# Kernel tuning notes

Measured on AMD Instinct MI355X. Metric: run time of the kernel, lower is better.

## Reference

```python
import jax, jax.numpy as jnp
import numpy as np

IN_DIM = 1024
QK_DIM = 64
NHEADS = 12
HN_MULT = 4
BATCH = 2
SEQ = 2048
BETA = 1.0 / np.sqrt(QK_DIM)


def setup_inputs() -> dict:
    key = jax.random.key(0)
    kg, kq, kk, kw = jax.random.split(key, 4)
    scale = 1.0 / np.sqrt(IN_DIM)
    g = jax.random.normal(kg, (BATCH, SEQ, IN_DIM), dtype=jnp.float32)
    Wq = jax.random.normal(kq, (NHEADS, QK_DIM, IN_DIM), dtype=jnp.float32) * scale
    Wk = jax.random.normal(kk, (NHEADS, QK_DIM, IN_DIM), dtype=jnp.float32) * scale
    Whn = jax.random.normal(kw, (HN_MULT * IN_DIM, IN_DIM), dtype=jnp.float32) * scale
    return {"g": g, "Wq": Wq, "Wk": Wk, "Whn": Whn}


def reference(g, Wq, Wk, Whn):
    # --- attention energy (Energy Transformer): E = -(1/beta) * sum logsumexp_keys(beta * q.k)
    q = jnp.einsum("bnd,hkd->bhnk", g, Wq)  # [B,H,N,K]
    k = jnp.einsum("bnd,hkd->bhnk", g, Wk)  # [B,H,N,K]
    scores = BETA * jnp.einsum("bhnk,bhmk->bhnm", q, k)  # [B,H,N(query),M(key)]
    e_attn = -(1.0 / BETA) * jnp.sum(jax.nn.logsumexp(scores, axis=-1))
    # --- Hopfield energy: -0.5 * sum(relu(W g)^2)
    h = jnp.einsum("bnd,md->bnm", g, Whn)  # [B,N,4*D]
    e_hn = -0.5 * jnp.sum(jax.nn.relu(h) ** 2)
    return e_attn + e_hn
```

## Files before the change

kernel.cpp:

```cpp
#include <hip/hip_runtime.h>
#include <hip/hip_bf16.h>

typedef __attribute__((ext_vector_type(4))) float f32x4;
typedef __attribute__((ext_vector_type(8))) short bf16x8;
typedef unsigned short u16;
typedef __attribute__((ext_vector_type(4))) u16 u16x4;


#define OFF_GB    ((size_t)0)
#define OFF_WQB   ((size_t)8388608)
#define OFF_WKB   ((size_t)(8388608+1572864))
#define OFF_WHNB  ((size_t)(8388608+2*1572864))
#define OFF_QB    (OFF_WHNB + 8388608)
#define OFF_KB    (OFF_QB + 6291456)

__device__ __forceinline__ u16 f2bf(float f) {
  union { float f; unsigned u; } x; x.f = f;
  unsigned u = x.u;
  u += 0x7fffu + ((u >> 16) & 1u);
  return (u16)(u >> 16);
}

__global__ __launch_bounds__(256) void convert_all(
    const float* __restrict__ g, const float* __restrict__ wq,
    const float* __restrict__ wk, const float* __restrict__ whn,
    u16* __restrict__ gB, u16* __restrict__ wqB, u16* __restrict__ wkB, u16* __restrict__ whnB)
{
  const int NG = 1048576;
  const int NW = 196608;
  const int total = NG + 2 * NW + NG;
  for (int i = blockIdx.x * blockDim.x + threadIdx.x; i < total; i += gridDim.x * blockDim.x) {
    const float4* src; u16* dst; int j; float scale = 1.0f;
    if (i < NG)              { src = (const float4*)g;   dst = gB;   j = i; }
    else if (i < NG + NW)    { src = (const float4*)wq;  dst = wqB;  j = i - NG;
                               scale = 0.125f * 1.44269504089f; }
    else if (i < NG + 2*NW)  { src = (const float4*)wk;  dst = wkB;  j = i - NG - NW; }
    else                     { src = (const float4*)whn; dst = whnB; j = i - NG - 2*NW; }
    float4 v = src[j];
    u16x4 o;
    o.x = f2bf(v.x * scale); o.y = f2bf(v.y * scale);
    o.z = f2bf(v.z * scale); o.w = f2bf(v.w * scale);
    *(u16x4*)(dst + (size_t)j * 4) = o;
  }
}

__global__ __launch_bounds__(256) void gemm_bt(
    const u16* __restrict__ A, const u16* __restrict__ B0, const u16* __restrict__ B1,
    u16* __restrict__ C0, u16* __restrict__ C1, int K)
{
  __shared__ u16 lA[128 * 64];
  __shared__ u16 lB[128 * 64];
  const int tid = threadIdx.x;
  const int lane = tid & 63;
  const int w = tid >> 6;
  const int bid = blockIdx.x;
  const int xcd = bid & 7, idx = bid >> 3;
  const int bm = ((xcd >> 1) << 3) + (idx & 7);
  const int bn = (xcd & 1) * 6 + (idx >> 3);

  const u16* Bp; u16* Cp; int bcol0;
  if (bn < 6) { Bp = B0; Cp = C0; bcol0 = bn * 128; }
  else        { Bp = B1; Cp = C1; bcol0 = (bn - 6) * 128; }
  const int arow0 = bm * 128;
  const int wr = w >> 1, wc = w & 1;
  const int l15 = lane & 15, lg = lane >> 4;

  f32x4 acc[4][4];
  const f32x4 zz = {0.f, 0.f, 0.f, 0.f};
#pragma unroll
  for (int m = 0; m < 4; m++)
#pragma unroll
    for (int n = 0; n < 4; n++) acc[m][n] = zz;

#define STAGE(KT) do {                                                                     \
    _Pragma("unroll")                                                                      \
    for (int i = 0; i < 4; i++) {                                                          \
      int rloc = w * 32 + i * 8 + (lane >> 3);                                             \
      int cb   = (((lane & 7) ^ (rloc & 7)) << 4);                                         \
      const char* srcA = (const char*)A + (((size_t)(arow0 + rloc)) * K + (KT) * 64) * 2 + cb; \
      __builtin_amdgcn_global_load_lds((const __attribute__((address_space(1))) void*)srcA, \
          (__attribute__((address_space(3))) void*)((char*)lA + (w * 32 + i * 8) * 128), 16, 0, 0); \
      const char* srcB = (const char*)Bp + (((size_t)(bcol0 + rloc)) * K + (KT) * 64) * 2 + cb; \
      __builtin_amdgcn_global_load_lds((const __attribute__((address_space(1))) void*)srcB, \
          (__attribute__((address_space(3))) void*)((char*)lB + (w * 32 + i * 8) * 128), 16, 0, 0); \
    }                                                                                      \
  } while (0)

  STAGE(0);
  const int nkt = K / 64;
  for (int kt = 0; kt < nkt; ++kt) {
    __syncthreads();
    bf16x8 a0[4], a1[4], b0[4], b1[4];
#pragma unroll
    for (int m = 0; m < 4; m++) {
      int row = wr * 64 + m * 16 + l15;
      const char* base = (const char*)lA + row * 128;
      int sw = (row & 7) << 4;
      a0[m] = *(const bf16x8*)(base + ((lg * 16) ^ sw));
      a1[m] = *(const bf16x8*)(base + ((64 + lg * 16) ^ sw));
    }
#pragma unroll
    for (int n = 0; n < 4; n++) {
      int row = wc * 64 + n * 16 + l15;
      const char* base = (const char*)lB + row * 128;
      int sw = (row & 7) << 4;
      b0[n] = *(const bf16x8*)(base + ((lg * 16) ^ sw));
      b1[n] = *(const bf16x8*)(base + ((64 + lg * 16) ^ sw));
    }
    __syncthreads();
    if (kt + 1 < nkt) STAGE(kt + 1);
#pragma unroll
    for (int m = 0; m < 4; m++)
#pragma unroll
      for (int n = 0; n < 4; n++) {
        acc[m][n] = __builtin_amdgcn_mfma_f32_16x16x32_bf16(a0[m], b0[n], acc[m][n], 0, 0, 0);
        acc[m][n] = __builtin_amdgcn_mfma_f32_16x16x32_bf16(a1[m], b1[n], acc[m][n], 0, 0, 0);
      }
  }
#pragma unroll
  for (int m = 0; m < 4; m++)
#pragma unroll
    for (int n = 0; n < 4; n++)
#pragma unroll
      for (int r = 0; r < 4; r++) {
        int row = arow0 + wr * 64 + m * 16 + lg * 4 + r;
        int col = bcol0 + wc * 64 + n * 16 + l15;
        size_t dst = ((((size_t)(row >> 11) * 12 + (col >> 6)) << 11) + (row & 2047)) * 64 + (col & 63);
        Cp[dst] = f2bf(acc[m][n][r]);
      }
#undef STAGE
}

__global__ __launch_bounds__(512, 2) void hop_gemm8(
    const u16* __restrict__ A, const u16* __restrict__ Bm, float* __restrict__ out)
{
  __shared__ __align__(16) u16 lds[2][2][2][128][64];
  const int tid = threadIdx.x;
  const int lane = tid & 63, w = tid >> 6;
  const int wr = w >> 2, wc = w & 3;
  const int l15 = lane & 15, lg = lane >> 4;
  const int bid = blockIdx.x;
  const int xcd = bid & 7, idx = bid >> 3;
  const int am0 = (((xcd >> 1) << 2) + (idx & 3)) * 256;
  const int bn0 = (((xcd & 1) << 3) + (idx >> 2)) * 256;
  constexpr int nkt = 16;

  f32x4 acc[8][4];
  const f32x4 zz = {0.f, 0.f, 0.f, 0.f};
#pragma unroll
  for (int i = 0; i < 8; i++)
#pragma unroll
    for (int j = 0; j < 4; j++) acc[i][j] = zz;

#define HSTAGE(KT, MAT, H) do {                                                            \
    const u16* s_ = (MAT) ? Bm : A;                                                        \
    int rb_ = ((MAT) ? bn0 : am0) + (H) * 128;                                             \
    char* d0_ = (char*)&lds[(KT) & 1][(MAT)][(H)][0][0];                                   \
    _Pragma("unroll")                                                                      \
    for (int q_ = 0; q_ < 2; q_++) {                                                       \
      int r_ = q_ * 64 + (tid >> 3);                                                       \
      int cb_ = ((tid & 7) * 16) ^ ((r_ & 7) << 4);                                        \
      const char* g_ = (const char*)s_ + (size_t)(rb_ + r_) * 2048 + (KT) * 128 + cb_;     \
      __builtin_amdgcn_global_load_lds((const __attribute__((address_space(1))) void*)g_,  \
          (__attribute__((address_space(3))) void*)(d0_ + q_ * 8192 + tid * 16), 16, 0, 0);\
    }                                                                                      \
  } while (0)

#define LDA_F(DST, P, I, S) do {                                                           \
    int rh_ = ((I) & 3) * 32 + wr * 16 + l15;                                              \
    const char* b_ = (const char*)&lds[(P)][0][(I) >> 2][0][0] + rh_ * 128;                \
    DST = *(const bf16x8*)(b_ + (((S) * 64 + lg * 16) ^ ((rh_ & 7) << 4)));                \
  } while (0)
#define LDB_F(DST, P, J, S) do {                                                           \
    int rh_ = ((J) & 1) * 64 + wc * 16 + l15;                                              \
    const char* b_ = (const char*)&lds[(P)][1][(J) >> 1][0][0] + rh_ * 128;                \
    DST = *(const bf16x8*)(b_ + (((S) * 64 + lg * 16) ^ ((rh_ & 7) << 4)));                \
  } while (0)

  HSTAGE(0, 0, 0); HSTAGE(0, 1, 0); HSTAGE(0, 1, 1); HSTAGE(0, 0, 1);
  HSTAGE(1, 0, 0); HSTAGE(1, 1, 0); HSTAGE(1, 1, 1);
  asm volatile("s_waitcnt vmcnt(6)" ::: "memory");
  __builtin_amdgcn_s_barrier();

  bf16x8 af[4][2], bf[4][2];

#pragma unroll 2
  for (int t = 0; t < nkt; ++t) {
    const int p = t & 1;
#pragma unroll
    for (int m = 0; m < 4; m++) { LDA_F(af[m][0], p, m, 0); LDA_F(af[m][1], p, m, 1); }
#pragma unroll
    for (int n = 0; n < 2; n++) { LDB_F(bf[n][0], p, n, 0); LDB_F(bf[n][1], p, n, 1); }
    if (t + 1 < nkt) HSTAGE(t + 1, 0, 1);
    __builtin_amdgcn_s_barrier();
    __builtin_amdgcn_s_setprio(1);
#pragma unroll
    for (int m = 0; m < 4; m++)
#pragma unroll
      for (int n = 0; n < 2; n++) {
        acc[m][n] = __builtin_amdgcn_mfma_f32_16x16x32_bf16(af[m][0], bf[n][0], acc[m][n], 0, 0, 0);
        acc[m][n] = __builtin_amdgcn_mfma_f32_16x16x32_bf16(af[m][1], bf[n][1], acc[m][n], 0, 0, 0);
      }
    __builtin_amdgcn_s_setprio(0);
    __builtin_amdgcn_s_barrier();
#pragma unroll
    for (int n = 2; n < 4; n++) { LDB_F(bf[n][0], p, n, 0); LDB_F(bf[n][1], p, n, 1); }
    if (t + 2 < nkt) HSTAGE(t + 2, 0, 0);
    __builtin_amdgcn_s_barrier();
    __builtin_amdgcn_s_setprio(1);
#pragma unroll
    for (int m = 0; m < 4; m++)
#pragma unroll
      for (int n = 2; n < 4; n++) {
        acc[m][n] = __builtin_amdgcn_mfma_f32_16x16x32_bf16(af[m][0], bf[n][0], acc[m][n], 0, 0, 0);
        acc[m][n] = __builtin_amdgcn_mfma_f32_16x16x32_bf16(af[m][1], bf[n][1], acc[m][n], 0, 0, 0);
      }
    __builtin_amdgcn_s_setprio(0);
    __builtin_amdgcn_s_barrier();
#pragma unroll
    for (int m = 0; m < 4; m++) { LDA_F(af[m][0], p, m + 4, 0); LDA_F(af[m][1], p, m + 4, 1); }
    if (t + 2 < nkt) HSTAGE(t + 2, 1, 0);
    __builtin_amdgcn_s_barrier();
    __builtin_amdgcn_s_setprio(1);
#pragma unroll
    for (int m = 0; m < 4; m++)
#pragma unroll
      for (int n = 2; n < 4; n++) {
        acc[m + 4][n] = __builtin_amdgcn_mfma_f32_16x16x32_bf16(af[m][0], bf[n][0], acc[m + 4][n], 0, 0, 0);
        acc[m + 4][n] = __builtin_amdgcn_mfma_f32_16x16x32_bf16(af[m][1], bf[n][1], acc[m + 4][n], 0, 0, 0);
      }
    __builtin_amdgcn_s_setprio(0);
    __builtin_amdgcn_s_barrier();
    if (t + 2 < nkt) HSTAGE(t + 2, 1, 1);
    __builtin_amdgcn_s_barrier();
    __builtin_amdgcn_s_setprio(1);
#pragma unroll
    for (int m = 0; m < 4; m++)
#pragma unroll
      for (int n = 0; n < 2; n++) {
        acc[m + 4][n] = __builtin_amdgcn_mfma_f32_16x16x32_bf16(af[m][0], bf[n][0], acc[m + 4][n], 0, 0, 0);
        acc[m + 4][n] = __builtin_amdgcn_mfma_f32_16x16x32_bf16(af[m][1], bf[n][1], acc[m + 4][n], 0, 0, 0);
      }
    __builtin_amdgcn_s_setprio(0);
    if (t < nkt - 2)       asm volatile("s_waitcnt vmcnt(6)" ::: "memory");
    else if (t == nkt - 2) asm volatile("s_waitcnt vmcnt(0)" ::: "memory");
    __builtin_amdgcn_s_barrier();
  }
#undef HSTAGE
#undef LDA_F
#undef LDB_F

  float loc = 0.f;
#pragma unroll
  for (int i = 0; i < 8; i++)
#pragma unroll
    for (int j = 0; j < 4; j++)
#pragma unroll
      for (int r = 0; r < 4; r++) {
        float v = acc[i][j][r];
        loc += (v > 0.f) ? v * v : 0.f;
      }
#pragma unroll
  for (int mask = 32; mask; mask >>= 1) loc += __shfl_xor(loc, mask, 64);
  if (lane == 0) atomicAdd(out, -0.5f * loc);
}

__global__ __launch_bounds__(256) void scores_lse(
    const u16* __restrict__ qB, const u16* __restrict__ kB, float* __restrict__ out)
{
  __shared__ __align__(16) u16 kbuf[3][128 * 64];
  const int z  = blockIdx.x;
  const int qt = blockIdx.y;
  const int tid = threadIdx.x, lane = tid & 63, w = tid >> 6;
  const int l15 = lane & 15, lg = lane >> 4;

  const u16* qp = qB + ((size_t)z * 2048 + qt * 64 + w * 16 + l15) * 64 + lg * 8;
  bf16x8 qf0 = *(const bf16x8*)qp;
  bf16x8 qf1 = *(const bf16x8*)(qp + 32);

#define KSTAGE(KB, BUF) do {                                                               \
    _Pragma("unroll")                                                                      \
    for (int i = 0; i < 4; i++) {                                                          \
      int rloc = i * 32 + w * 8 + (lane >> 3);                                             \
      int cb   = (((lane & 7) ^ (rloc & 7)) << 4);                                         \
      const char* src = (const char*)kB + ((size_t)z * 2048 + (KB) * 128 + rloc) * 128 + cb; \
      __builtin_amdgcn_global_load_lds((const __attribute__((address_space(1))) void*)src,  \
          (__attribute__((address_space(3))) void*)((char*)kbuf[(BUF)] + rloc * 128 + (lane & 7) * 16), 16, 0, 0); \
    }                                                                                      \
  } while (0)

  f32x4 sacc = {0.f, 0.f, 0.f, 0.f};
  const f32x4 zz = {0.f, 0.f, 0.f, 0.f};

  KSTAGE(0, 0);
  KSTAGE(1, 1);
  asm volatile("s_waitcnt vmcnt(4)" ::: "memory");
  __builtin_amdgcn_s_barrier();
  __builtin_amdgcn_sched_barrier(0);

  const int NKB = 16;
  for (int kb = 0; kb < NKB; ++kb) {
    if (kb + 2 < NKB) KSTAGE(kb + 2, (kb + 2) % 3);
    const char* cur = (const char*)kbuf[kb % 3];
#pragma unroll
    for (int g2 = 0; g2 < 8; ++g2) {
      int row = g2 * 16 + l15;
      const char* base = cur + row * 128;
      int sw = (row & 7) << 4;
      bf16x8 b0 = *(const bf16x8*)(base + ((lg * 16) ^ sw));
      bf16x8 b1 = *(const bf16x8*)(base + ((64 + lg * 16) ^ sw));
      f32x4 s = zz;
      s = __builtin_amdgcn_mfma_f32_16x16x32_bf16(qf0, b0, s, 0, 0, 0);
      s = __builtin_amdgcn_mfma_f32_16x16x32_bf16(qf1, b1, s, 0, 0, 0);
      sacc[0] += __builtin_amdgcn_exp2f(s[0]);
      sacc[1] += __builtin_amdgcn_exp2f(s[1]);
      sacc[2] += __builtin_amdgcn_exp2f(s[2]);
      sacc[3] += __builtin_amdgcn_exp2f(s[3]);
    }
    if (kb + 1 < NKB) {
      if (kb + 2 < NKB) asm volatile("s_waitcnt vmcnt(4)" ::: "memory");
      else              asm volatile("s_waitcnt vmcnt(0)" ::: "memory");
      __builtin_amdgcn_s_barrier();
      __builtin_amdgcn_sched_barrier(0);
    }
  }
#undef KSTAGE

#pragma unroll
  for (int mask = 8; mask; mask >>= 1) {
    sacc[0] += __shfl_xor(sacc[0], mask, 64);
    sacc[1] += __shfl_xor(sacc[1], mask, 64);
    sacc[2] += __shfl_xor(sacc[2], mask, 64);
    sacc[3] += __shfl_xor(sacc[3], mask, 64);
  }
  float part = 0.f;
  if (l15 == 0) {
    part = __builtin_amdgcn_logf(sacc[0]) + __builtin_amdgcn_logf(sacc[1]) +
           __builtin_amdgcn_logf(sacc[2]) + __builtin_amdgcn_logf(sacc[3]);
  }
  part += __shfl_xor(part, 16, 64);
  part += __shfl_xor(part, 32, 64);
  if (lane == 0) atomicAdd(out, -5.5451774444795625f * part);
}

extern "C" void kernel_launch(void* const* d_in, const int* in_sizes, int n_in,
                              void* d_out, int out_size, void* d_ws, size_t ws_size,
                              hipStream_t stream)
{
  const float* g   = (const float*)d_in[0];
  const float* Wq  = (const float*)d_in[1];
  const float* Wk  = (const float*)d_in[2];
  const float* Whn = (const float*)d_in[3];
  float* out = (float*)d_out;
  char* ws = (char*)d_ws;

  u16* gB   = (u16*)(ws + OFF_GB);
  u16* wqB  = (u16*)(ws + OFF_WQB);
  u16* wkB  = (u16*)(ws + OFF_WKB);
  u16* whnB = (u16*)(ws + OFF_WHNB);
  u16* qB   = (u16*)(ws + OFF_QB);
  u16* kB   = (u16*)(ws + OFF_KB);

  (void)hipMemsetAsync(out, 0, sizeof(float), stream);

  convert_all<<<2048, 256, 0, stream>>>(g, Wq, Wk, Whn, gB, wqB, wkB, whnB);
  gemm_bt<<<384, 256, 0, stream>>>(gB, wqB, wkB, qB, kB, 1024);
  hop_gemm8<<<256, 512, 0, stream>>>(gB, whnB, out);
  scores_lse<<<dim3(24, 32), 256, 0, stream>>>(qB, kB, out);
}
```

Before: 205.6 us.

## Restructure Hopfield GEMM to 256x128 tiles with 3-stage single-barrier pipeline

Replaces the 256x256 tile, 8-wave ping-pong Hopfield GEMM with a 256x128 tile using K-step 32 and a triple-buffered LDS ring with one barrier per iteration. The grid doubles to 512 blocks and each wave holds half as many accumulators, so launch bounds ask for 4 blocks per CU. The aim is to cut barrier overhead and raise occupancy to hide latency. In exchange, arithmetic intensity per block drops and global/L2 traffic for A roughly doubles.

```diff
diff --git a/kernel.cpp b/kernel.cpp
--- a/kernel.cpp
+++ b/kernel.cpp
@@ -131,133 +131,91 @@
 #undef STAGE
 }
 
-__global__ __launch_bounds__(512, 2) void hop_gemm8(
+__global__ __launch_bounds__(512, 4) void hop_gemm(
     const u16* __restrict__ A, const u16* __restrict__ Bm, float* __restrict__ out)
 {
-  __shared__ __align__(16) u16 lds[2][2][2][128][64];
+  __shared__ __align__(16) u16 lds[3][(256 + 128) * 32];
   const int tid = threadIdx.x;
   const int lane = tid & 63, w = tid >> 6;
-  const int wr = w >> 2, wc = w & 3;
+  const int wr = w >> 1, wc = w & 1;
   const int l15 = lane & 15, lg = lane >> 4;
   const int bid = blockIdx.x;
   const int xcd = bid & 7, idx = bid >> 3;
   const int am0 = (((xcd >> 1) << 2) + (idx & 3)) * 256;
-  const int bn0 = (((xcd & 1) << 3) + (idx >> 2)) * 256;
-  constexpr int nkt = 16;
-
-  f32x4 acc[8][4];
+  const int bn0 = (((xcd & 1) << 4) + (idx >> 2)) * 128;
+  constexpr int nkt = 32;
+
+  f32x4 acc[4][4];
   const f32x4 zz = {0.f, 0.f, 0.f, 0.f};
 #pragma unroll
-  for (int i = 0; i < 8; i++)
-#pragma unroll
-    for (int j = 0; j < 4; j++) acc[i][j] = zz;
-
-#define HSTAGE(KT, MAT, H) do {                                                            \
-    const u16* s_ = (MAT) ? Bm : A;                                                        \
-    int rb_ = ((MAT) ? bn0 : am0) + (H) * 128;                                             \
-    char* d0_ = (char*)&lds[(KT) & 1][(MAT)][(H)][0][0];                                   \
+  for (int m = 0; m < 4; m++)
+#pragma unroll
+    for (int n = 0; n < 4; n++) acc[m][n] = zz;
+
+#define HSTAGE(KT) do {                                                                    \
+    char* s0_ = (char*)&lds[(KT) % 3][0];                                                  \
     _Pragma("unroll")                                                                      \
-    for (int q_ = 0; q_ < 2; q_++) {                                                       \
-      int r_ = q_ * 64 + (tid >> 3);                                                       \
-      int cb_ = ((tid & 7) * 16) ^ ((r_ & 7) << 4);                                        \
-      const char* g_ = (const char*)s_ + (size_t)(rb_ + r_) * 2048 + (KT) * 128 + cb_;     \
+    for (int i_ = 0; i_ < 2; i_++) {                                                       \
+      int r_ = i_ * 128 + (tid >> 2);                                                      \
+      int cb_ = ((tid & 3) * 16) ^ ((r_ & 3) << 4);                                        \
+      const char* g_ = (const char*)A + (size_t)(am0 + r_) * 2048 + (KT) * 64 + cb_;       \
       __builtin_amdgcn_global_load_lds((const __attribute__((address_space(1))) void*)g_,  \
-          (__attribute__((address_space(3))) void*)(d0_ + q_ * 8192 + tid * 16), 16, 0, 0);\
+          (__attribute__((address_space(3))) void*)(s0_ + i_ * 8192 + tid * 16), 16, 0, 0);\
     }                                                                                      \
-  } while (0)
-
-#define LDA_F(DST, P, I, S) do {                                                           \
-    int rh_ = ((I) & 3) * 32 + wr * 16 + l15;                                              \
-    const char* b_ = (const char*)&lds[(P)][0][(I) >> 2][0][0] + rh_ * 128;                \
-    DST = *(const bf16x8*)(b_ + (((S) * 64 + lg * 16) ^ ((rh_ & 7) << 4)));                \
-  } while (0)
-#define LDB_F(DST, P, J, S) do {                                                           \
-    int rh_ = ((J) & 1) * 64 + wc * 16 + l15;                                              \
-    const char* b_ = (const char*)&lds[(P)][1][(J) >> 1][0][0] + rh_ * 128;                \
-    DST = *(const bf16x8*)(b_ + (((S) * 64 + lg * 16) ^ ((rh_ & 7) << 4)));                \
-  } while (0)
-
-  HSTAGE(0, 0, 0); HSTAGE(0, 1, 0); HSTAGE(0, 1, 1); HSTAGE(0, 0, 1);
-  HSTAGE(1, 0, 0); HSTAGE(1, 1, 0); HSTAGE(1, 1, 1);
-  asm volatile("s_waitcnt vmcnt(6)" ::: "memory");
+    {                                                                                      \
+      int r_ = tid >> 2;                                                                   \
+      int cb_ = ((tid & 3) * 16) ^ ((r_ & 3) << 4);                                        \
+      const char* g_ = (const char*)Bm + (size_t)(bn0 + r_) * 2048 + (KT) * 64 + cb_;      \
+      __builtin_amdgcn_global_load_lds((const __attribute__((address_space(1))) void*)g_,  \
+          (__attribute__((address_space(3))) void*)(s0_ + 16384 + tid * 16), 16, 0, 0);    \
+    }                                                                                      \
+  } while (0)
+
+#define LDA2(DST, SL, M) do {                                                              \
+    int r_ = wr * 64 + (M) * 16 + l15;                                                     \
+    DST = *(const bf16x8*)((const char*)&lds[(SL)][0] + r_ * 64 + ((lg * 16) ^ ((r_ & 3) << 4))); \
+  } while (0)
+#define LDB2(DST, SL, N) do {                                                              \
+    int r_ = wc * 64 + (N) * 16 + l15;                                                     \
+    DST = *(const bf16x8*)((const char*)&lds[(SL)][0] + 16384 + r_ * 64 + ((lg * 16) ^ ((r_ & 3) << 4))); \
+  } while (0)
+
+  HSTAGE(0);
+  HSTAGE(1);
+  asm volatile("s_waitcnt vmcnt(3)" ::: "memory");
   __builtin_amdgcn_s_barrier();
 
-  bf16x8 af[4][2], bf[4][2];
-
-#pragma unroll 2
   for (int t = 0; t < nkt; ++t) {
-    const int p = t & 1;
-#pragma unroll
-    for (int m = 0; m < 4; m++) { LDA_F(af[m][0], p, m, 0); LDA_F(af[m][1], p, m, 1); }
-#pragma unroll
-    for (int n = 0; n < 2; n++) { LDB_F(bf[n][0], p, n, 0); LDB_F(bf[n][1], p, n, 1); }
-    if (t + 1 < nkt) HSTAGE(t + 1, 0, 1);
-    __builtin_amdgcn_s_barrier();
+    const int sl = t % 3;
+    if (t + 2 < nkt) HSTAGE(t + 2);
+    bf16x8 av[4], bv[4];
+#pragma unroll
+    for (int m = 0; m < 4; m++) LDA2(av[m], sl, m);
+#pragma unroll
+    for (int n = 0; n < 4; n++) LDB2(bv[n], sl, n);
     __builtin_amdgcn_s_setprio(1);
 #pragma unroll
     for (int m = 0; m < 4; m++)
 #pragma unroll
-      for (int n = 0; n < 2; n++) {
-        acc[m][n] = __builtin_amdgcn_mfma_f32_16x16x32_bf16(af[m][0], bf[n][0], acc[m][n], 0, 0, 0);
-        acc[m][n] = __builtin_amdgcn_mfma_f32_16x16x32_bf16(af[m][1], bf[n][1], acc[m][n], 0, 0, 0);
-      }
+      for (int n = 0; n < 4; n++)
+        acc[m][n] = __builtin_amdgcn_mfma_f32_16x16x32_bf16(av[m], bv[n], acc[m][n], 0, 0, 0);
     __builtin_amdgcn_s_setprio(0);
-    __builtin_amdgcn_s_barrier();
-#pragma unroll
-    for (int n = 2; n < 4; n++) { LDB_F(bf[n][0], p, n, 0); LDB_F(bf[n][1], p, n, 1); }
-    if (t + 2 < nkt) HSTAGE(t + 2, 0, 0);
-    __builtin_amdgcn_s_barrier();
-    __builtin_amdgcn_s_setprio(1);
-#pragma unroll
-    for (int m = 0; m < 4; m++)
-#pragma unroll
-      for (int n = 2; n < 4; n++) {
-        acc[m][n] = __builtin_amdgcn_mfma_f32_16x16x32_bf16(af[m][0], bf[n][0], acc[m][n], 0, 0, 0);
-        acc[m][n] = __builtin_amdgcn_mfma_f32_16x16x32_bf16(af[m][1], bf[n][1], acc[m][n], 0, 0, 0);
-      }
-    __builtin_amdgcn_s_setprio(0);
-    __builtin_amdgcn_s_barrier();
-#pragma unroll
-    for (int m = 0; m < 4; m++) { LDA_F(af[m][0], p, m + 4, 0); LDA_F(af[m][1], p, m + 4, 1); }
-    if (t + 2 < nkt) HSTAGE(t + 2, 1, 0);
-    __builtin_amdgcn_s_barrier();
-    __builtin_amdgcn_s_setprio(1);
-#pragma unroll
-    for (int m = 0; m < 4; m++)
-#pragma unroll
-      for (int n = 2; n < 4; n++) {
-        acc[m + 4][n] = __builtin_amdgcn_mfma_f32_16x16x32_bf16(af[m][0], bf[n][0], acc[m + 4][n], 0, 0, 0);
-        acc[m + 4][n] = __builtin_amdgcn_mfma_f32_16x16x32_bf16(af[m][1], bf[n][1], acc[m + 4][n], 0, 0, 0);
-      }
-    __builtin_amdgcn_s_setprio(0);
-    __builtin_amdgcn_s_barrier();
-    if (t + 2 < nkt) HSTAGE(t + 2, 1, 1);
-    __builtin_amdgcn_s_barrier();
-    __builtin_amdgcn_s_setprio(1);
-#pragma unroll
-    for (int m = 0; m < 4; m++)
-#pragma unroll
-      for (int n = 0; n < 2; n++) {
-        acc[m + 4][n] = __builtin_amdgcn_mfma_f32_16x16x32_bf16(af[m][0], bf[n][0], acc[m + 4][n], 0, 0, 0);
-        acc[m + 4][n] = __builtin_amdgcn_mfma_f32_16x16x32_bf16(af[m][1], bf[n][1], acc[m + 4][n], 0, 0, 0);
-      }
-    __builtin_amdgcn_s_setprio(0);
-    if (t < nkt - 2)       asm volatile("s_waitcnt vmcnt(6)" ::: "memory");
-    else if (t == nkt - 2) asm volatile("s_waitcnt vmcnt(0)" ::: "memory");
-    __builtin_amdgcn_s_barrier();
+    if (t + 2 < nkt)      asm volatile("s_waitcnt vmcnt(3)" ::: "memory");
+    else if (t + 1 < nkt) asm volatile("s_waitcnt vmcnt(0)" ::: "memory");
+    if (t + 1 < nkt) __builtin_amdgcn_s_barrier();
   }
 #undef HSTAGE
-#undef LDA_F
-#undef LDB_F
+#undef LDA2
+#undef LDB2
 
   float loc = 0.f;
 #pragma unroll
-  for (int i = 0; i < 8; i++)
-#pragma unroll
-    for (int j = 0; j < 4; j++)
+  for (int m = 0; m < 4; m++)
+#pragma unroll
+    for (int n = 0; n < 4; n++)
 #pragma unroll
       for (int r = 0; r < 4; r++) {
-        float v = acc[i][j][r];
+        float v = acc[m][n][r];
         loc += (v > 0.f) ? v * v : 0.f;
       }
 #pragma unroll
@@ -365,6 +323,6 @@
 
   convert_all<<<2048, 256, 0, stream>>>(g, Wq, Wk, Whn, gB, wqB, wkB, whnB);
   gemm_bt<<<384, 256, 0, stream>>>(gB, wqB, wkB, qB, kB, 1024);
-  hop_gemm8<<<256, 512, 0, stream>>>(gB, whnB, out);
+  hop_gemm<<<512, 512, 0, stream>>>(gB, whnB, out);
   scores_lse<<<dim3(24, 32), 256, 0, stream>>>(qB, kB, out);
 }
```

Measured after the change: 230.0 us. +11.9%, slower.
